# Kernel optimization log

Hardware: AMD Instinct MI355X
Metric: run time of the kernel (lower is better)

Reference implementation:

```python
import jax, jax.numpy as jnp
import numpy as np

N, QLEN, KLEN = 4, 2048, 2048
QDIM = KVDIM = 512
EMBED, HEADS = 1024, 16
HEAD_DIM = EMBED // HEADS


def setup_inputs() -> dict:
    key = jax.random.key(0)
    ks = jax.random.split(key, 7)
    return {
        "queries": jax.random.normal(ks[0], (N, QLEN, QDIM), dtype=jnp.float32),
        "keys": jax.random.normal(ks[1], (1, KLEN, KVDIM), dtype=jnp.float32),
        "values": jax.random.normal(ks[2], (1, KLEN, KVDIM), dtype=jnp.float32),
        "mask": jax.random.randint(ks[3], (N, 1, 1, KLEN), 0, 2, dtype=jnp.int32),
        "Wq": jax.random.normal(ks[4], (QDIM, EMBED), dtype=jnp.float32) * (QDIM ** -0.5),
        "Wk": jax.random.normal(ks[5], (KVDIM, EMBED), dtype=jnp.float32) * (KVDIM ** -0.5),
        "Wv": jax.random.normal(ks[6], (KVDIM, EMBED), dtype=jnp.float32) * (KVDIM ** -0.5),
    }


def reference(queries, keys, values, mask, Wq, Wk, Wv):
    # Projections (Linear, no bias)
    q = (queries @ Wq).reshape(N, QLEN, HEADS, HEAD_DIM)      # [N, Q, H, D]
    k = (keys @ Wk).reshape(KLEN, HEADS, HEAD_DIM)            # [K, H, D] (batch-1, shared)
    v = (values @ Wv).reshape(KLEN, HEADS, HEAD_DIM)          # [K, H, D]

    # energy: [N, H, Q, K]
    energy = jnp.einsum('nqhd,khd->nhqk', q, k)
    energy = jnp.where(mask == 0, jnp.float32(-1e20), energy)
    attn = jax.nn.softmax(energy / jnp.float32(HEAD_DIM ** 0.5), axis=3)

    out = jnp.einsum('nhqk,khd->nqhd', attn, v)               # [N, Q, H, D]
    return out.reshape(N, QLEN, EMBED)
```

## Files before the change

kernel.cpp:

```cpp
#include <hip/hip_runtime.h>

#define NB 4
#define QLEN 2048
#define KLEN 2048
#define QDIM 512
#define EMBED 1024
#define HEADS 16
#define HD 64

typedef __bf16 bf16x8 __attribute__((ext_vector_type(8)));
typedef float f32x4 __attribute__((ext_vector_type(4)));
typedef float f32x16 __attribute__((ext_vector_type(16)));

#define CLOG 0.18033688011112042f

__device__ __forceinline__ float fexp2(float x) {
#if __has_builtin(__builtin_amdgcn_exp2f)
    return __builtin_amdgcn_exp2f(x);
#else
    float r;
    asm("v_exp_f32 %0, %1\n\ts_nop 1" : "=v"(r) : "v"(x));
    return r;
#endif
}

#if __has_builtin(__builtin_amdgcn_sched_barrier)
#define SCHED_FENCE() __builtin_amdgcn_sched_barrier(0)
#else
#define SCHED_FENCE()
#endif

__device__ __forceinline__ void dma16(const void* g, void* l) {
    __builtin_amdgcn_global_load_lds(
        (const __attribute__((address_space(1))) void*)g,
        (__attribute__((address_space(3))) void*)l, 16, 0, 0);
}

__global__ __launch_bounds__(256) void prep(const float* __restrict__ q,
                                            const float* __restrict__ k,
                                            const float* __restrict__ v,
                                            const float* __restrict__ Wq,
                                            const float* __restrict__ Wk,
                                            const float* __restrict__ Wv,
                                            __bf16* __restrict__ qd,
                                            __bf16* __restrict__ kd,
                                            __bf16* __restrict__ vd,
                                            __bf16* __restrict__ WtQ,
                                            __bf16* __restrict__ WtK,
                                            __bf16* __restrict__ WtV) {
    __shared__ float tile[32][33];
    int b = blockIdx.x, tid = threadIdx.x;
    if (b < 3072) {
        const float* src; __bf16* dst; int cb;
        if (b < 2048)      { src = q; dst = qd; cb = b; }
        else if (b < 2560) { src = k; dst = kd; cb = b - 2048; }
        else               { src = v; dst = vd; cb = b - 2560; }
        int i = (cb * 256 + tid) * 8;
        float4 a0 = *(const float4*)&src[i];
        float4 a1 = *(const float4*)&src[i + 4];
        bf16x8 o;
        o[0] = (__bf16)a0.x; o[1] = (__bf16)a0.y; o[2] = (__bf16)a0.z; o[3] = (__bf16)a0.w;
        o[4] = (__bf16)a1.x; o[5] = (__bf16)a1.y; o[6] = (__bf16)a1.z; o[7] = (__bf16)a1.w;
        *(bf16x8*)&dst[i] = o;
    } else {
        int tb = b - 3072;
        int which = tb >> 9, r = tb & 511;
        const float* src = (which == 0) ? Wq : (which == 1) ? Wk : Wv;
        __bf16* dst = (which == 0) ? WtQ : (which == 1) ? WtK : WtV;
        float scale = (which == 0) ? CLOG : 1.0f;
        int e0 = (r & 31) * 32, c0 = (r >> 5) * 32;
        int tx = tid & 31, ty = tid >> 5;
        for (int i = 0; i < 4; i++)
            tile[ty + 8 * i][tx] = src[(c0 + ty + 8 * i) * EMBED + e0 + tx];
        __syncthreads();
        for (int i = 0; i < 4; i++)
            dst[(e0 + ty + 8 * i) * QDIM + c0 + tx] = (__bf16)(tile[tx][ty + 8 * i] * scale);
    }
}

__device__ __forceinline__ void gemm_compute(const __bf16* As, const __bf16* Bs,
                                             int wr, int wc, int r16, int qq,
                                             f32x4 (&acc)[4][4]) {
    bf16x8 af[4], bq[4];
#pragma unroll
    for (int i = 0; i < 4; i++)
        af[i] = *(const bf16x8*)&As[(wr * 64 + i * 16 + r16) * 32 + qq * 8];
#pragma unroll
    for (int j = 0; j < 4; j++)
        bq[j] = *(const bf16x8*)&Bs[(wc * 64 + j * 16 + r16) * 32 + qq * 8];
#pragma unroll
    for (int i = 0; i < 4; i++)
#pragma unroll
        for (int j = 0; j < 4; j++)
            acc[i][j] = __builtin_amdgcn_mfma_f32_16x16x32_bf16(af[i], bq[j], acc[i][j], 0, 0, 0);
}

__device__ __forceinline__ void gemm128(const __bf16* __restrict__ A,
                                        const __bf16* __restrict__ Bt,
                                        __bf16* As0, __bf16* As1,
                                        __bf16* Bs0, __bf16* Bs1,
                                        int row0, int col0, f32x4 (&acc)[4][4]) {
    int tid = threadIdx.x, wave = tid >> 6, lane = tid & 63;
    int r16 = lane & 15, qq = lane >> 4;
    int wr = wave >> 1, wc = wave & 1;
    const __bf16* agp1 = A + (size_t)(row0 + (tid >> 2)) * QDIM + (tid & 3) * 8;
    const __bf16* agp2 = A + (size_t)(row0 + 64 + (tid >> 2)) * QDIM + (tid & 3) * 8;
    const __bf16* bgp1 = Bt + (size_t)(col0 + (tid >> 2)) * QDIM + (tid & 3) * 8;
    const __bf16* bgp2 = Bt + (size_t)(col0 + 64 + (tid >> 2)) * QDIM + (tid & 3) * 8;
    __bf16 *a0a = &As0[wave * 512], *a0b = &As0[2048 + wave * 512];
    __bf16 *a1a = &As1[wave * 512], *a1b = &As1[2048 + wave * 512];
    __bf16 *b0a = &Bs0[wave * 512], *b0b = &Bs0[2048 + wave * 512];
    __bf16 *b1a = &Bs1[wave * 512], *b1b = &Bs1[2048 + wave * 512];

    dma16(agp1, a0a); dma16(agp2, a0b);
    dma16(bgp1, b0a); dma16(bgp2, b0b);
    agp1 += 32; agp2 += 32; bgp1 += 32; bgp2 += 32;
    __syncthreads();

    for (int t = 0; t < 16; t += 2) {
        dma16(agp1, a1a); dma16(agp2, a1b);
        dma16(bgp1, b1a); dma16(bgp2, b1b);
        agp1 += 32; agp2 += 32; bgp1 += 32; bgp2 += 32;
        SCHED_FENCE();
        gemm_compute(As0, Bs0, wr, wc, r16, qq, acc);
        __syncthreads();
        if (t + 2 < 16) {
            dma16(agp1, a0a); dma16(agp2, a0b);
            dma16(bgp1, b0a); dma16(bgp2, b0b);
            agp1 += 32; agp2 += 32; bgp1 += 32; bgp2 += 32;
        }
        SCHED_FENCE();
        gemm_compute(As1, Bs1, wr, wc, r16, qq, acc);
        __syncthreads();
    }
}

__global__ __launch_bounds__(256) void proj_all(const __bf16* __restrict__ qin,
                                                const __bf16* __restrict__ kin,
                                                const __bf16* __restrict__ vin,
                                                const __bf16* __restrict__ wtq,
                                                const __bf16* __restrict__ wtk,
                                                const __bf16* __restrict__ wtv,
                                                __bf16* __restrict__ qout,
                                                __bf16* __restrict__ kout,
                                                __bf16* __restrict__ vtout) {
    __shared__ __align__(16) __bf16 As[2][128 * 32];
    __shared__ __align__(16) __bf16 Bs[2][128 * 32];
    int bid = blockIdx.x;
    const __bf16 *A, *Bt;
    int mode, b;
    if (bid < 512)      { A = qin; Bt = wtq; mode = 0; b = bid; }
    else if (bid < 640) { A = kin; Bt = wtk; mode = 1; b = bid - 512; }
    else                { A = vin; Bt = wtv; mode = 2; b = bid - 640; }
    int row0 = (b >> 3) * 128, col0 = (b & 7) * 128;
    f32x4 acc[4][4] = {};
    gemm128(A, Bt, As[0], As[1], Bs[0], Bs[1], row0, col0, acc);
    int lane = threadIdx.x & 63, wave = threadIdx.x >> 6;
    int r16 = lane & 15, qq = lane >> 4;
    int wr = wave >> 1, wc = wave & 1;
#pragma unroll
    for (int i = 0; i < 4; i++)
#pragma unroll
        for (int j = 0; j < 4; j++)
#pragma unroll
            for (int rr = 0; rr < 4; rr++) {
                int grow = row0 + wr * 64 + i * 16 + qq * 4 + rr;
                int gcol = col0 + wc * 64 + j * 16 + r16;
                int hh = gcol >> 6, d = gcol & 63;
                __bf16 v = (__bf16)acc[i][j][rr];
                if (mode == 0) {
                    int n = grow >> 11, qr = grow & 2047;
                    qout[((size_t)(n * HEADS + hh) * QLEN + qr) * HD + d] = v;
                } else if (mode == 1) {
                    kout[((size_t)hh * KLEN + grow) * HD + d] = v;
                } else {
                    vtout[((size_t)hh * HD + d) * KLEN + grow] = v;
                }
            }
}

__device__ __forceinline__ void attn_tile(const __bf16* ksb, const __bf16* vsb,
                                          const float* mrow, const bf16x8 (&qfrag)[4],
                                          int col, int h,
                                          f32x16& o0, f32x16& o1, float& rsl) {
    bf16x8 pfrag[4];
#pragma unroll
    for (int kt2 = 0; kt2 < 2; kt2++) {
        int R = kt2 * 32 + col;
        f32x16 s = {};
#pragma unroll
        for (int c = 0; c < 4; c++) {
            int cc = (2 * c + h) ^ (R & 7);
            bf16x8 kf = *(const bf16x8*)&ksb[(R * 8 + cc) * 8];
            s = __builtin_amdgcn_mfma_f32_32x32x16_bf16(kf, qfrag[c], s, 0, 0, 0);
        }
#pragma unroll
        for (int G = 0; G < 4; G++) {
            f32x4 mt = *(const f32x4*)&mrow[kt2 * 32 + 16 * (G >> 1) + 8 * h + 4 * (G & 1)];
            int ci = 2 * kt2 + (G >> 1), e0 = (G & 1) * 4;
#pragma unroll
            for (int rr = 0; rr < 4; rr++) {
                float p = fexp2(s[4 * G + rr] + mt[rr]);
                rsl += p;
                pfrag[ci][e0 + rr] = (__bf16)p;
            }
        }
    }
#pragma unroll
    for (int c = 0; c < 4; c++) {
        int cc = (2 * c + h) ^ (col & 7);
        bf16x8 v0 = *(const bf16x8*)&vsb[(col * 8 + cc) * 8];
        bf16x8 v1 = *(const bf16x8*)&vsb[((32 + col) * 8 + cc) * 8];
        o0 = __builtin_amdgcn_mfma_f32_32x32x16_bf16(v0, pfrag[c], o0, 0, 0, 0);
        o1 = __builtin_amdgcn_mfma_f32_32x32x16_bf16(v1, pfrag[c], o1, 0, 0, 0);
    }
}

__global__ __launch_bounds__(256, 4) void attn_kernel(const __bf16* __restrict__ qb,
                                                      const __bf16* __restrict__ kb,
                                                      const __bf16* __restrict__ vtb,
                                                      const int* __restrict__ mask,
                                                      float* __restrict__ out) {
    __shared__ __align__(16) __bf16 ks[2][4096];
    __shared__ __align__(16) __bf16 vs[2][4096];
    __shared__ __align__(16) float msf[KLEN];

    int tid = threadIdx.x, wave = tid >> 6, lane = tid & 63;
    int col = lane & 31, h = lane >> 5;
    int q0 = blockIdx.x * 128, hh = blockIdx.y, n = blockIdx.z;
    const __bf16* qg = qb + ((size_t)(n * HEADS + hh) * QLEN + q0 + wave * 32 + col) * HD;
    const __bf16* kg = kb + (size_t)hh * KLEN * HD;
    const __bf16* vg = vtb + (size_t)hh * HD * KLEN;
    const int* mg = mask + n * KLEN;

    bf16x8 qfrag[4];
#pragma unroll
    for (int c = 0; c < 4; c++) qfrag[c] = *(const bf16x8*)&qg[c * 16 + h * 8];

    int s1 = tid, R1 = s1 >> 3, c1 = (s1 & 7) ^ (R1 & 7);
    int s2 = tid + 256, R2 = s2 >> 3, c2 = (s2 & 7) ^ (R2 & 7);
    int g1 = (R1 & 0x33) | ((R1 & 4) << 1) | ((R1 & 8) >> 1);
    int g2 = (R2 & 0x33) | ((R2 & 4) << 1) | ((R2 & 8) >> 1);
    const __bf16* kgp1 = kg + g1 * HD + c1 * 8;
    const __bf16* kgp2 = kg + g2 * HD + c2 * 8;
    const __bf16* vgp1 = vg + (size_t)R1 * KLEN + c1 * 8;
    const __bf16* vgp2 = vg + (size_t)R2 * KLEN + c2 * 8;
    __bf16 *kl0a = &ks[0][wave * 512], *kl0b = &ks[0][2048 + wave * 512];
    __bf16 *kl1a = &ks[1][wave * 512], *kl1b = &ks[1][2048 + wave * 512];
    __bf16 *vl0a = &vs[0][wave * 512], *vl0b = &vs[0][2048 + wave * 512];
    __bf16 *vl1a = &vs[1][wave * 512], *vl1b = &vs[1][2048 + wave * 512];

    dma16(kgp1, kl0a); dma16(kgp2, kl0b);
    dma16(vgp1, vl0a); dma16(vgp2, vl0b);
    kgp1 += 64 * HD; kgp2 += 64 * HD; vgp1 += 64; vgp2 += 64;
    {
        int i8 = tid * 8;
        int4 ma = *(const int4*)&mg[i8];
        int4 mb = *(const int4*)&mg[i8 + 4];
        f32x4 fa, fb;
        fa[0] = ma.x ? 0.f : -1e30f; fa[1] = ma.y ? 0.f : -1e30f;
        fa[2] = ma.z ? 0.f : -1e30f; fa[3] = ma.w ? 0.f : -1e30f;
        fb[0] = mb.x ? 0.f : -1e30f; fb[1] = mb.y ? 0.f : -1e30f;
        fb[2] = mb.z ? 0.f : -1e30f; fb[3] = mb.w ? 0.f : -1e30f;
        *(f32x4*)&msf[i8] = fa;
        *(f32x4*)&msf[i8 + 4] = fb;
    }
    __syncthreads();

    f32x16 o0 = {}, o1 = {};
    float rsl = 0.f;

    for (int t = 0; t < 32; t += 2) {
        dma16(kgp1, kl1a); dma16(kgp2, kl1b);
        dma16(vgp1, vl1a); dma16(vgp2, vl1b);
        kgp1 += 64 * HD; kgp2 += 64 * HD; vgp1 += 64; vgp2 += 64;
        SCHED_FENCE();
        attn_tile(ks[0], vs[0], &msf[t * 64], qfrag, col, h, o0, o1, rsl);
        __syncthreads();
        if (t + 2 < 32) {
            dma16(kgp1, kl0a); dma16(kgp2, kl0b);
            dma16(vgp1, vl0a); dma16(vgp2, vl0b);
            kgp1 += 64 * HD; kgp2 += 64 * HD; vgp1 += 64; vgp2 += 64;
        }
        SCHED_FENCE();
        attn_tile(ks[1], vs[1], &msf[(t + 1) * 64], qfrag, col, h, o0, o1, rsl);
        __syncthreads();
    }

    rsl += __shfl_xor(rsl, 32);
    float inv = 1.0f / rsl;
    float* op = out + ((size_t)n * QLEN + q0 + wave * 32 + col) * EMBED + hh * HD;
#pragma unroll
    for (int G = 0; G < 4; G++) {
        float4 t0, t1;
        t0.x = o0[4 * G + 0] * inv; t0.y = o0[4 * G + 1] * inv;
        t0.z = o0[4 * G + 2] * inv; t0.w = o0[4 * G + 3] * inv;
        t1.x = o1[4 * G + 0] * inv; t1.y = o1[4 * G + 1] * inv;
        t1.z = o1[4 * G + 2] * inv; t1.w = o1[4 * G + 3] * inv;
        *(float4*)&op[8 * G + 4 * h] = t0;
        *(float4*)&op[32 + 8 * G + 4 * h] = t1;
    }
}

extern "C" void kernel_launch(void* const* d_in, const int* in_sizes, int n_in,
                              void* d_out, int out_size, void* d_ws, size_t ws_size,
                              hipStream_t stream) {
    const float* queries = (const float*)d_in[0];
    const float* keys    = (const float*)d_in[1];
    const float* values  = (const float*)d_in[2];
    const int*   mask    = (const int*)d_in[3];
    const float* Wq      = (const float*)d_in[4];
    const float* Wk      = (const float*)d_in[5];
    const float* Wv      = (const float*)d_in[6];
    float* out = (float*)d_out;

    const size_t MiB = 1048576;
    char* ws = (char*)d_ws;
    __bf16* qbf   = (__bf16*)(ws);
    __bf16* kbf   = (__bf16*)(ws + 16 * MiB);
    __bf16* vtbf  = (__bf16*)(ws + 20 * MiB);
    __bf16* wtq   = (__bf16*)(ws + 24 * MiB);
    __bf16* wtk   = (__bf16*)(ws + 25 * MiB);
    __bf16* wtv   = (__bf16*)(ws + 26 * MiB);
    __bf16* qin   = (__bf16*)(ws + 27 * MiB);
    __bf16* kin   = (__bf16*)(ws + 35 * MiB);
    __bf16* vin   = (__bf16*)(ws + 37 * MiB);

    prep<<<4608, 256, 0, stream>>>(queries, keys, values, Wq, Wk, Wv,
                                   qin, kin, vin, wtq, wtk, wtv);
    proj_all<<<768, 256, 0, stream>>>(qin, kin, vin, wtq, wtk, wtv, qbf, kbf, vtbf);
    attn_kernel<<<dim3(QLEN / 128, HEADS, NB), 256, 0, stream>>>(qbf, kbf, vtbf, mask, out);
}
```

Before: 189.4 us.

## Precompute multiplicative mask, stage V-transpose via LDS, pack bf16 conversions

```diff
diff --git a/kernel.cpp b/kernel.cpp
--- a/kernel.cpp
+++ b/kernel.cpp
@@ -24,6 +24,22 @@
 #endif
 }
 
+#if __has_builtin(__builtin_amdgcn_cvt_pk_bf16_f32)
+typedef __bf16 bf16x2_t __attribute__((ext_vector_type(2)));
+__device__ __forceinline__ unsigned pack_bf16(float a, float b) {
+    bf16x2_t r = __builtin_amdgcn_cvt_pk_bf16_f32(a, b);
+    return __builtin_bit_cast(unsigned, r);
+}
+#else
+__device__ __forceinline__ unsigned pack_bf16(float a, float b) {
+    unsigned ua = __builtin_bit_cast(unsigned, a);
+    unsigned ub = __builtin_bit_cast(unsigned, b);
+    ua = (ua + 0x7FFFu + ((ua >> 16) & 1u)) >> 16;
+    ub = (ub + 0x7FFFu + ((ub >> 16) & 1u)) & 0xFFFF0000u;
+    return ua | ub;
+}
+#endif
+
 #if __has_builtin(__builtin_amdgcn_sched_barrier)
 #define SCHED_FENCE() __builtin_amdgcn_sched_barrier(0)
 #else
@@ -42,12 +58,14 @@
                                             const float* __restrict__ Wq,
                                             const float* __restrict__ Wk,
                                             const float* __restrict__ Wv,
+                                            const int* __restrict__ mask,
                                             __bf16* __restrict__ qd,
                                             __bf16* __restrict__ kd,
                                             __bf16* __restrict__ vd,
                                             __bf16* __restrict__ WtQ,
                                             __bf16* __restrict__ WtK,
-                                            __bf16* __restrict__ WtV) {
+                                            __bf16* __restrict__ WtV,
+                                            float* __restrict__ mskf) {
     __shared__ float tile[32][33];
     int b = blockIdx.x, tid = threadIdx.x;
     if (b < 3072) {
@@ -62,7 +80,7 @@
         o[0] = (__bf16)a0.x; o[1] = (__bf16)a0.y; o[2] = (__bf16)a0.z; o[3] = (__bf16)a0.w;
         o[4] = (__bf16)a1.x; o[5] = (__bf16)a1.y; o[6] = (__bf16)a1.z; o[7] = (__bf16)a1.w;
         *(bf16x8*)&dst[i] = o;
-    } else {
+    } else if (b < 4608) {
         int tb = b - 3072;
         int which = tb >> 9, r = tb & 511;
         const float* src = (which == 0) ? Wq : (which == 1) ? Wk : Wv;
@@ -75,6 +93,17 @@
         __syncthreads();
         for (int i = 0; i < 4; i++)
             dst[(e0 + ty + 8 * i) * QDIM + c0 + tx] = (__bf16)(tile[tx][ty + 8 * i] * scale);
+    } else {
+        int i = ((b - 4608) * 256 + tid) * 8;
+        int4 ma = *(const int4*)&mask[i];
+        int4 mb = *(const int4*)&mask[i + 4];
+        f32x4 fa, fb;
+        fa[0] = ma.x ? 1.f : 0.f; fa[1] = ma.y ? 1.f : 0.f;
+        fa[2] = ma.z ? 1.f : 0.f; fa[3] = ma.w ? 1.f : 0.f;
+        fb[0] = mb.x ? 1.f : 0.f; fb[1] = mb.y ? 1.f : 0.f;
+        fb[2] = mb.z ? 1.f : 0.f; fb[3] = mb.w ? 1.f : 0.f;
+        *(f32x4*)&mskf[i] = fa;
+        *(f32x4*)&mskf[i + 4] = fb;
     }
 }
 
@@ -144,8 +173,7 @@
                                                 __bf16* __restrict__ qout,
                                                 __bf16* __restrict__ kout,
                                                 __bf16* __restrict__ vtout) {
-    __shared__ __align__(16) __bf16 As[2][128 * 32];
-    __shared__ __align__(16) __bf16 Bs[2][128 * 32];
+    __shared__ __align__(16) __bf16 pool[16640];
     int bid = blockIdx.x;
     const __bf16 *A, *Bt;
     int mode, b;
@@ -154,56 +182,86 @@
     else                { A = vin; Bt = wtv; mode = 2; b = bid - 640; }
     int row0 = (b >> 3) * 128, col0 = (b & 7) * 128;
     f32x4 acc[4][4] = {};
-    gemm128(A, Bt, As[0], As[1], Bs[0], Bs[1], row0, col0, acc);
-    int lane = threadIdx.x & 63, wave = threadIdx.x >> 6;
+    gemm128(A, Bt, &pool[0], &pool[4096], &pool[8192], &pool[12288], row0, col0, acc);
+    int tid = threadIdx.x;
+    int lane = tid & 63, wave = tid >> 6;
     int r16 = lane & 15, qq = lane >> 4;
     int wr = wave >> 1, wc = wave & 1;
-#pragma unroll
-    for (int i = 0; i < 4; i++)
-#pragma unroll
-        for (int j = 0; j < 4; j++)
-#pragma unroll
-            for (int rr = 0; rr < 4; rr++) {
-                int grow = row0 + wr * 64 + i * 16 + qq * 4 + rr;
-                int gcol = col0 + wc * 64 + j * 16 + r16;
-                int hh = gcol >> 6, d = gcol & 63;
-                __bf16 v = (__bf16)acc[i][j][rr];
-                if (mode == 0) {
-                    int n = grow >> 11, qr = grow & 2047;
-                    qout[((size_t)(n * HEADS + hh) * QLEN + qr) * HD + d] = v;
-                } else if (mode == 1) {
-                    kout[((size_t)hh * KLEN + grow) * HD + d] = v;
-                } else {
-                    vtout[((size_t)hh * HD + d) * KLEN + grow] = v;
+    if (mode < 2) {
+#pragma unroll
+        for (int i = 0; i < 4; i++)
+#pragma unroll
+            for (int j = 0; j < 4; j++)
+#pragma unroll
+                for (int rr = 0; rr < 4; rr++) {
+                    int grow = row0 + wr * 64 + i * 16 + qq * 4 + rr;
+                    int gcol = col0 + wc * 64 + j * 16 + r16;
+                    int hh = gcol >> 6, d = gcol & 63;
+                    __bf16 v = (__bf16)acc[i][j][rr];
+                    if (mode == 0) {
+                        int n = grow >> 11, qr = grow & 2047;
+                        qout[((size_t)(n * HEADS + hh) * QLEN + qr) * HD + d] = v;
+                    } else {
+                        kout[((size_t)hh * KLEN + grow) * HD + d] = v;
+                    }
+                }
+    } else {
+#pragma unroll
+        for (int i = 0; i < 4; i++)
+#pragma unroll
+            for (int j = 0; j < 4; j++) {
+                int orow = wc * 64 + j * 16 + r16;
+#pragma unroll
+                for (int rr = 0; rr < 4; rr++) {
+                    int ocol = wr * 64 + i * 16 + qq * 4 + rr;
+                    pool[orow * 130 + ocol] = (__bf16)acc[i][j][rr];
                 }
             }
+        __syncthreads();
+        int orow = tid >> 1, kh = (tid & 1) * 64;
+        int hh = (col0 >> 6) + (orow >> 6), d = orow & 63;
+        const __bf16* lp = &pool[orow * 130 + kh];
+        __bf16* gp = vtout + ((size_t)hh * HD + d) * KLEN + row0 + kh;
+#pragma unroll
+        for (int jj = 0; jj < 8; jj++)
+            *(uint4*)&gp[jj * 8] = *(const uint4*)&lp[jj * 8];
+    }
 }
 
 __device__ __forceinline__ void attn_tile(const __bf16* ksb, const __bf16* vsb,
-                                          const float* mrow, const bf16x8 (&qfrag)[4],
+                                          const float* __restrict__ mrow,
+                                          const bf16x8 (&qfrag)[4], const f32x16& zro,
                                           int col, int h,
-                                          f32x16& o0, f32x16& o1, float& rsl) {
-    bf16x8 pfrag[4];
+                                          f32x16& o0, f32x16& o1, float2& rsl) {
+    uint4 pf[4];
 #pragma unroll
     for (int kt2 = 0; kt2 < 2; kt2++) {
         int R = kt2 * 32 + col;
-        f32x16 s = {};
-#pragma unroll
-        for (int c = 0; c < 4; c++) {
+        f32x16 s;
+        {
+            int cc = h ^ (R & 7);
+            bf16x8 kf = *(const bf16x8*)&ksb[(R * 8 + cc) * 8];
+            s = __builtin_amdgcn_mfma_f32_32x32x16_bf16(kf, qfrag[0], zro, 0, 0, 0);
+        }
+#pragma unroll
+        for (int c = 1; c < 4; c++) {
             int cc = (2 * c + h) ^ (R & 7);
             bf16x8 kf = *(const bf16x8*)&ksb[(R * 8 + cc) * 8];
             s = __builtin_amdgcn_mfma_f32_32x32x16_bf16(kf, qfrag[c], s, 0, 0, 0);
         }
 #pragma unroll
         for (int G = 0; G < 4; G++) {
-            f32x4 mt = *(const f32x4*)&mrow[kt2 * 32 + 16 * (G >> 1) + 8 * h + 4 * (G & 1)];
-            int ci = 2 * kt2 + (G >> 1), e0 = (G & 1) * 4;
-#pragma unroll
-            for (int rr = 0; rr < 4; rr++) {
-                float p = fexp2(s[4 * G + rr] + mt[rr]);
-                rsl += p;
-                pfrag[ci][e0 + rr] = (__bf16)p;
-            }
+            f32x4 mv = *(const f32x4*)&mrow[kt2 * 32 + 16 * (G >> 1) + 8 * h + 4 * (G & 1)];
+            float p0 = fexp2(s[4 * G + 0]) * mv[0];
+            float p1 = fexp2(s[4 * G + 1]) * mv[1];
+            float p2 = fexp2(s[4 * G + 2]) * mv[2];
+            float p3 = fexp2(s[4 * G + 3]) * mv[3];
+            rsl.x += p0 + p2;
+            rsl.y += p1 + p3;
+            unsigned lo = pack_bf16(p0, p1), hi = pack_bf16(p2, p3);
+            int ci = 2 * kt2 + (G >> 1);
+            if ((G & 1) == 0) { pf[ci].x = lo; pf[ci].y = hi; }
+            else              { pf[ci].z = lo; pf[ci].w = hi; }
         }
     }
 #pragma unroll
@@ -211,19 +269,19 @@
         int cc = (2 * c + h) ^ (col & 7);
         bf16x8 v0 = *(const bf16x8*)&vsb[(col * 8 + cc) * 8];
         bf16x8 v1 = *(const bf16x8*)&vsb[((32 + col) * 8 + cc) * 8];
-        o0 = __builtin_amdgcn_mfma_f32_32x32x16_bf16(v0, pfrag[c], o0, 0, 0, 0);
-        o1 = __builtin_amdgcn_mfma_f32_32x32x16_bf16(v1, pfrag[c], o1, 0, 0, 0);
+        bf16x8 pb = __builtin_bit_cast(bf16x8, pf[c]);
+        o0 = __builtin_amdgcn_mfma_f32_32x32x16_bf16(v0, pb, o0, 0, 0, 0);
+        o1 = __builtin_amdgcn_mfma_f32_32x32x16_bf16(v1, pb, o1, 0, 0, 0);
     }
 }
 
 __global__ __launch_bounds__(256, 4) void attn_kernel(const __bf16* __restrict__ qb,
                                                       const __bf16* __restrict__ kb,
                                                       const __bf16* __restrict__ vtb,
-                                                      const int* __restrict__ mask,
+                                                      const float* __restrict__ mskf,
                                                       float* __restrict__ out) {
     __shared__ __align__(16) __bf16 ks[2][4096];
     __shared__ __align__(16) __bf16 vs[2][4096];
-    __shared__ __align__(16) float msf[KLEN];
 
     int tid = threadIdx.x, wave = tid >> 6, lane = tid & 63;
     int col = lane & 31, h = lane >> 5;
@@ -231,7 +289,7 @@
     const __bf16* qg = qb + ((size_t)(n * HEADS + hh) * QLEN + q0 + wave * 32 + col) * HD;
     const __bf16* kg = kb + (size_t)hh * KLEN * HD;
     const __bf16* vg = vtb + (size_t)hh * HD * KLEN;
-    const int* mg = mask + n * KLEN;
+    const float* mbase = mskf + n * KLEN;
 
     bf16x8 qfrag[4];
 #pragma unroll
@@ -253,29 +311,18 @@
     dma16(kgp1, kl0a); dma16(kgp2, kl0b);
     dma16(vgp1, vl0a); dma16(vgp2, vl0b);
     kgp1 += 64 * HD; kgp2 += 64 * HD; vgp1 += 64; vgp2 += 64;
-    {
-        int i8 = tid * 8;
-        int4 ma = *(const int4*)&mg[i8];
-        int4 mb = *(const int4*)&mg[i8 + 4];
-        f32x4 fa, fb;
-        fa[0] = ma.x ? 0.f : -1e30f; fa[1] = ma.y ? 0.f : -1e30f;
-        fa[2] = ma.z ? 0.f : -1e30f; fa[3] = ma.w ? 0.f : -1e30f;
-        fb[0] = mb.x ? 0.f : -1e30f; fb[1] = mb.y ? 0.f : -1e30f;
-        fb[2] = mb.z ? 0.f : -1e30f; fb[3] = mb.w ? 0.f : -1e30f;
-        *(f32x4*)&msf[i8] = fa;
-        *(f32x4*)&msf[i8 + 4] = fb;
-    }
     __syncthreads();
 
     f32x16 o0 = {}, o1 = {};
-    float rsl = 0.f;
+    const f32x16 zro = {};
+    float2 rsl = {0.f, 0.f};
 
     for (int t = 0; t < 32; t += 2) {
         dma16(kgp1, kl1a); dma16(kgp2, kl1b);
         dma16(vgp1, vl1a); dma16(vgp2, vl1b);
         kgp1 += 64 * HD; kgp2 += 64 * HD; vgp1 += 64; vgp2 += 64;
         SCHED_FENCE();
-        attn_tile(ks[0], vs[0], &msf[t * 64], qfrag, col, h, o0, o1, rsl);
+        attn_tile(ks[0], vs[0], mbase + t * 64, qfrag, zro, col, h, o0, o1, rsl);
         __syncthreads();
         if (t + 2 < 32) {
             dma16(kgp1, kl0a); dma16(kgp2, kl0b);
@@ -283,12 +330,13 @@
             kgp1 += 64 * HD; kgp2 += 64 * HD; vgp1 += 64; vgp2 += 64;
         }
         SCHED_FENCE();
-        attn_tile(ks[1], vs[1], &msf[(t + 1) * 64], qfrag, col, h, o0, o1, rsl);
-        __syncthreads();
-    }
-
-    rsl += __shfl_xor(rsl, 32);
-    float inv = 1.0f / rsl;
+        attn_tile(ks[1], vs[1], mbase + (t + 1) * 64, qfrag, zro, col, h, o0, o1, rsl);
+        __syncthreads();
+    }
+
+    float r = rsl.x + rsl.y;
+    r += __shfl_xor(r, 32);
+    float inv = 1.0f / r;
     float* op = out + ((size_t)n * QLEN + q0 + wave * 32 + col) * EMBED + hh * HD;
 #pragma unroll
     for (int G = 0; G < 4; G++) {
@@ -325,9 +373,10 @@
     __bf16* qin   = (__bf16*)(ws + 27 * MiB);
     __bf16* kin   = (__bf16*)(ws + 35 * MiB);
     __bf16* vin   = (__bf16*)(ws + 37 * MiB);
-
-    prep<<<4608, 256, 0, stream>>>(queries, keys, values, Wq, Wk, Wv,
-                                   qin, kin, vin, wtq, wtk, wtv);
+    float*  mskf  = (float*)(ws + 39 * MiB);
+
+    prep<<<4612, 256, 0, stream>>>(queries, keys, values, Wq, Wk, Wv, mask,
+                                   qin, kin, vin, wtq, wtk, wtv, mskf);
     proj_all<<<768, 256, 0, stream>>>(qin, kin, vin, wtq, wtk, wtv, qbf, kbf, vtbf);
-    attn_kernel<<<dim3(QLEN / 128, HEADS, NB), 256, 0, stream>>>(qbf, kbf, vtbf, mask, out);
-}
+    attn_kernel<<<dim3(QLEN / 128, HEADS, NB), 256, 0, stream>>>(qbf, kbf, vtbf, mskf, out);
+}
```

Measured after the change: 218.6 us. 1.15x slower.
